# Performance work log

Hardware: AMD Instinct MI355X
Metric: run time of the kernel (lower is better)

The kernel has to match this reference:

```python
import jax, jax.numpy as jnp
import numpy as np

V, E, H, L = 32000, 512, 512, 3
HI = 2 * H  # expansion_factor = 2
B, S = 16, 2048


def setup_inputs() -> dict:
    key = jax.random.key(0)
    ks = jax.random.split(key, 9)
    x_source = jax.random.randint(ks[0], (B, S), 1, V)
    x_lengths = jax.random.randint(ks[1], (B,), 1, S + 1)
    x_lengths = x_lengths.at[0].set(S)  # ensure max(x_lengths) == S so truncation is static
    emb = jax.random.normal(ks[2], (V, E), jnp.float32) * 0.02
    emb = emb.at[0].set(0.0)  # padding_idx=0
    W_er = jax.random.normal(ks[3], (E, H), jnp.float32) / np.sqrt(E)
    b_er = jnp.zeros((H,), jnp.float32)
    W_hg_fwd = jax.random.normal(ks[4], (L, H, 2 * HI), jnp.float32) / np.sqrt(H)
    W_out_fwd = jax.random.normal(ks[5], (L, HI, H), jnp.float32) / np.sqrt(HI)
    W_hg_rev = jax.random.normal(ks[6], (L, H, 2 * HI), jnp.float32) / np.sqrt(H)
    W_out_rev = jax.random.normal(ks[7], (L, HI, H), jnp.float32) / np.sqrt(HI)
    return {"x_source": x_source, "x_lengths": x_lengths, "emb": emb,
            "W_er": W_er, "b_er": b_er,
            "W_hg_fwd": W_hg_fwd, "W_out_fwd": W_out_fwd,
            "W_hg_rev": W_hg_rev, "W_out_rev": W_out_rev}


def _log_g(x):
    # log of g(x) = where(x>=0, x+0.5, sigmoid(x)), computed stably in log space
    return jnp.where(x >= 0, jnp.log(jax.nn.relu(x) + 0.5), -jax.nn.softplus(-x))


def _mingru(x, W_hg, W_out):
    # x: [B,S,H] -> [B,S,H]; parallel minGRU via Heinsen associative scan in log space
    hidden, gate = jnp.split(x @ W_hg, 2, axis=-1)  # each [B,S,HI]
    log_coeffs = -jax.nn.softplus(gate)             # log(1 - z)
    log_values = -jax.nn.softplus(-gate) + _log_g(hidden)  # log z + log g(h~)
    a_star = jnp.cumsum(log_coeffs, axis=1)
    log_h = a_star + jax.lax.cumlogsumexp(log_values - a_star, axis=1)
    return jnp.exp(log_h) @ W_out


def _circ_shift_left(x, pad):
    # per-sample left rotation by pad[i]: cat([x[i, pad:], x[i, :pad]])
    Sl = x.shape[1]
    idx = (jnp.arange(Sl)[None, :] + pad[:, None]) % Sl  # [B,S]
    return jnp.take_along_axis(x, idx[:, :, None], axis=1)


def reference(x_source, x_lengths, emb, W_er, b_er, W_hg_fwd, W_out_fwd, W_hg_rev, W_out_rev):
    # seq_length = max(x_lengths) == S by construction, so truncation is identity
    x_emb = emb[x_source] @ W_er + b_er            # [B,S,H]
    pad = x_emb.shape[1] - x_lengths               # [B]
    rev = _circ_shift_left(jnp.flip(x_emb, axis=1), pad)
    h, hr = x_emb, rev
    for i in range(W_hg_fwd.shape[0]):
        h = _mingru(h, W_hg_fwd[i], W_out_fwd[i])
        hr = _mingru(hr, W_hg_rev[i], W_out_rev[i])
    hr = _circ_shift_left(jnp.flip(hr, axis=1), pad)
    out = jnp.concatenate([h, hr], axis=-1)        # [B,S,2H]
    # flattened gather in original == out[i, x_lengths[i]-1]
    seq_h = out[jnp.arange(out.shape[0]), x_lengths - 1]  # [B,2H]
    return out, seq_h
```

## Files before the change

### kernel.cpp

```cpp
#include <hip/hip_runtime.h>
#include <hip/hip_bf16.h>
#include <stdint.h>

#define S_LEN  2048
#define BATCH  16
#define HDIM   512
#define HIDIM  1024
#define NLAYER 3
#define SCAN_C 32
#define SCAN_T 64

typedef __hip_bfloat16 bf16;
typedef __attribute__((ext_vector_type(8))) short bf16x8;
typedef __attribute__((ext_vector_type(4))) float f32x4;
typedef unsigned int u32;

#define GLOAD16(gp, lp) __builtin_amdgcn_global_load_lds(                 \
    (const __attribute__((address_space(1))) void*)(gp),                  \
    (__attribute__((address_space(3))) void*)(lp), 16, 0, 0)

#define FENCE asm volatile("" ::: "memory")
#define BAR   do { FENCE; __builtin_amdgcn_s_barrier(); FENCE; } while (0)
#define VMCNT(n) asm volatile("s_waitcnt vmcnt(" #n ")" ::: "memory")

__global__ void probe_dtype(const unsigned short* __restrict__ w, int* __restrict__ flag)
{
  int cnt = 0;
  for (int i = threadIdx.x; i < 4096; i += 64) {
    unsigned short m = w[i] & 0x7FFF;
    if (m > 0x4080) cnt++;
  }
  for (int o = 32; o; o >>= 1) cnt += __shfl_down(cnt, o, 64);
  if (threadIdx.x == 0) *flag = (cnt > 64) ? 1 : 0;
}

__device__ __forceinline__ void av_calc(float hid, float gate, float& a, float& v) {
  a = 1.0f / (1.0f + __expf(gate));
  float z = 1.0f / (1.0f + __expf(-gate));
  float g = (hid >= 0.0f) ? (hid + 0.5f) : (1.0f / (1.0f + __expf(-hid)));
  v = z * g;
}

__device__ __forceinline__ short f2bs(float f) {
  bf16 h = (bf16)f;
  return *(short*)&h;
}

__device__ __forceinline__ bf16x8 pack8(float4 a, float4 b) {
  bf16x8 r;
  r[0] = f2bs(a.x); r[1] = f2bs(a.y); r[2] = f2bs(a.z); r[3] = f2bs(a.w);
  r[4] = f2bs(b.x); r[5] = f2bs(b.y); r[6] = f2bs(b.z); r[7] = f2bs(b.w);
  return r;
}


__device__ __forceinline__ void stage_half(const bf16* __restrict__ G, int row0, int ld,
                                           int kbase, char* lhalf, int tid)
{
  const int r  = tid >> 3;
  const int cc = (((tid & 7) ^ ((tid >> 3) & 7)) << 3);
  const bf16* g0 = G + (long)(row0 + r) * ld + (kbase + cc);
  char* l = lhalf + ((tid >> 6) << 10);
  GLOAD16(g0, l);
  GLOAD16(g0 + (long)64 * ld, l + 8192);
}

__device__ __forceinline__ bf16x8 frag_ld(const char* base, int Rl, int cb) {
  return *(const bf16x8*)(base + Rl * 128 + (cb ^ ((Rl & 7) << 4)));
}

__global__ __launch_bounds__(512, 2)
void gemm8(const bf16* __restrict__ A, const bf16* __restrict__ Bt,
           bf16* __restrict__ Cout, int K, int lda, int ldc)
{
  extern __shared__ char lds[];

  const int tid  = threadIdx.x;
  const int wave = tid >> 6;
  const int lane = tid & 63;
  const int wm = wave >> 2;
  const int wn = wave & 3;

  const u32 nwg = gridDim.x * gridDim.y;
  const u32 hb  = blockIdx.y * gridDim.x + blockIdx.x;
  const u32 cpx = nwg >> 3;
  const u32 swz = (hb & 7u) * cpx + (hb >> 3);
  const int m0 = (int)(swz / gridDim.x) * 256;
  const int n0 = (int)(swz % gridDim.x) * 256;

  char* A0 = lds;
  char* B0 = lds + 32768;
  char* A1 = lds + 65536;
  char* B1 = lds + 98304;

  const int fr = lane & 15;
  const int qh = lane >> 4;
  const int cqh = qh * 16;

  f32x4 acc[8][4];
#pragma unroll
  for (int i = 0; i < 8; i++)
#pragma unroll
    for (int j = 0; j < 4; j++)
#pragma unroll
      for (int r = 0; r < 4; r++) acc[i][j][r] = 0.0f;

  const int NJ = K >> 7;

  stage_half(A,  m0,       lda, 0,  A0,         tid);
  stage_half(A,  m0 + 128, lda, 0,  A0 + 16384, tid);
  stage_half(Bt, n0,       K,   0,  B0,         tid);
  stage_half(Bt, n0 + 128, K,   0,  B0 + 16384, tid);
  stage_half(Bt, n0,       K,   64, B1,         tid);
  stage_half(Bt, n0 + 128, K,   64, B1 + 16384, tid);
  VMCNT(4);
  BAR;

  for (int j = 0; j < NJ; ++j) {
    const int last = (j == NJ - 1);
    const int kO  = (2 * j + 1) * 64;
    const int kE2 = (2 * j + 2) * 64;
    const int kO2 = (2 * j + 3) * 64;

    {
      bf16x8 bfrag[4][2];
#pragma unroll
      for (int q = 0; q < 4; ++q) {
        if (q == 0) {
#pragma unroll
          for (int nt = 0; nt < 4; ++nt)
#pragma unroll
            for (int kk = 0; kk < 2; ++kk)
              bfrag[nt][kk] = frag_ld(B0, wn * 64 + nt * 16 + fr, kk * 64 + cqh);
        }
        bf16x8 afrag[2][2];
#pragma unroll
        for (int t = 0; t < 2; ++t)
#pragma unroll
          for (int kk = 0; kk < 2; ++kk)
            afrag[t][kk] = frag_ld(A0, wm * 128 + (2 * q + t) * 16 + fr, kk * 64 + cqh);

        if (q == 0) {
          stage_half(A, m0,       lda, kO, A1,         tid);
          stage_half(A, m0 + 128, lda, kO, A1 + 16384, tid);
        } else if (q == 1) {
          if (!last) stage_half(Bt, n0,       K, kE2, B0,         tid);
        } else if (q == 2) {
          if (!last) stage_half(Bt, n0 + 128, K, kE2, B0 + 16384, tid);
        }

        BAR;
        __builtin_amdgcn_s_setprio(1);
#pragma unroll
        for (int t = 0; t < 2; ++t)
#pragma unroll
          for (int nt = 0; nt < 4; ++nt)
#pragma unroll
            for (int kk = 0; kk < 2; ++kk)
              acc[2 * q + t][nt] = __builtin_amdgcn_mfma_f32_16x16x32_bf16(
                  afrag[t][kk], bfrag[nt][kk], acc[2 * q + t][nt], 0, 0, 0);
        __builtin_amdgcn_s_setprio(0);
        if (q == 3) {
          if (last) { VMCNT(0); } else { VMCNT(4); }
        }
        BAR;
      }
    }

    {
      bf16x8 bfrag[4][2];
#pragma unroll
      for (int q = 0; q < 4; ++q) {
        if (q == 0) {
#pragma unroll
          for (int nt = 0; nt < 4; ++nt)
#pragma unroll
            for (int kk = 0; kk < 2; ++kk)
              bfrag[nt][kk] = frag_ld(B1, wn * 64 + nt * 16 + fr, kk * 64 + cqh);
        }
        bf16x8 afrag[2][2];
#pragma unroll
        for (int t = 0; t < 2; ++t)
#pragma unroll
          for (int kk = 0; kk < 2; ++kk)
            afrag[t][kk] = frag_ld(A1, wm * 128 + (2 * q + t) * 16 + fr, kk * 64 + cqh);

        if (!last) {
          if (q == 0)      stage_half(A,  m0,       lda, kE2, A0,         tid);
          else if (q == 1) stage_half(A,  m0 + 128, lda, kE2, A0 + 16384, tid);
          else if (q == 2) stage_half(Bt, n0,       K,   kO2, B1,         tid);
          else             stage_half(Bt, n0 + 128, K,   kO2, B1 + 16384, tid);
        }

        BAR;
        __builtin_amdgcn_s_setprio(1);
#pragma unroll
        for (int t = 0; t < 2; ++t)
#pragma unroll
          for (int nt = 0; nt < 4; ++nt)
#pragma unroll
            for (int kk = 0; kk < 2; ++kk)
              acc[2 * q + t][nt] = __builtin_amdgcn_mfma_f32_16x16x32_bf16(
                  afrag[t][kk], bfrag[nt][kk], acc[2 * q + t][nt], 0, 0, 0);
        __builtin_amdgcn_s_setprio(0);
        if (q == 3 && !last) { VMCNT(4); }
        BAR;
      }
    }
  }

  const int orow = qh * 4;
#pragma unroll
  for (int mt = 0; mt < 8; ++mt) {
#pragma unroll
    for (int nt = 0; nt < 4; ++nt) {
      int gr = m0 + wm * 128 + mt * 16 + orow;
      int gc = n0 + wn * 64 + nt * 16 + fr;
#pragma unroll
      for (int r = 0; r < 4; ++r)
        Cout[(long)(gr + r) * ldc + gc] = (bf16)acc[mt][nt][r];
    }
  }
}

template<int GATHER, int BIAS>
__global__ __launch_bounds__(256, 2)
void gemm_mfma(const void* __restrict__ Av, const bf16* __restrict__ Bt,
               bf16* __restrict__ Cout, const float* __restrict__ bias,
               const int* __restrict__ gidx, const int* __restrict__ flag,
               int M, int N, int K, int lda, int ldc)
{
  __shared__ bf16 As[128 * 32];
  __shared__ bf16 Bs[128 * 32];

  const int tid  = threadIdx.x;
  const int wave = tid >> 6;
  const int lane = tid & 63;
  const int m0 = blockIdx.y * 128;
  const int n0 = blockIdx.x * 128;

  const int seg0 = wave * 2, seg1 = seg0 + 1;
  const int lr = lane >> 2;
  const int ck = (lane & 3) * 8;
  const int rA0 = seg0 * 16 + lr;
  const int rA1 = seg1 * 16 + lr;

  const int af = GATHER ? *flag : 0;

  long ga0 = GATHER ? (long)gidx[m0 + rA0] : (long)(m0 + rA0);
  long ga1 = GATHER ? (long)gidx[m0 + rA1] : (long)(m0 + rA1);
  const bf16*  hA0 = (const bf16*)Av + ga0 * (long)lda + ck;
  const bf16*  hA1 = (const bf16*)Av + ga1 * (long)lda + ck;
  const float* qA0 = (const float*)Av + ga0 * (long)lda + ck;
  const float* qA1 = (const float*)Av + ga1 * (long)lda + ck;
  const bf16*  pB0 = Bt + (long)(n0 + rA0) * K + ck;
  const bf16*  pB1 = Bt + (long)(n0 + rA1) * K + ck;

  bf16* lA0 = &As[seg0 * 512 + lane * 8];
  bf16* lA1 = &As[seg1 * 512 + lane * 8];
  bf16* lB0 = &Bs[seg0 * 512 + lane * 8];
  bf16* lB1 = &Bs[seg1 * 512 + lane * 8];

  f32x4 acc[4][4];
#pragma unroll
  for (int i = 0; i < 4; i++)
#pragma unroll
    for (int j = 0; j < 4; j++)
#pragma unroll
      for (int r = 0; r < 4; r++) acc[i][j][r] = 0.0f;

  const int mBase = (wave >> 1) * 64;
  const int nBase = (wave & 1) * 64;
  const int fr = lane & 15;
  const int fq = (lane >> 4) * 8;

  for (int k0 = 0; k0 < K; k0 += 32) {
    bf16x8 va0, va1;
    if (GATHER && af) {
      float4 a0 = *(const float4*)(qA0 + k0);
      float4 a1 = *(const float4*)(qA0 + k0 + 4);
      float4 b0 = *(const float4*)(qA1 + k0);
      float4 b1 = *(const float4*)(qA1 + k0 + 4);
      va0 = pack8(a0, a1);
      va1 = pack8(b0, b1);
    } else {
      va0 = *(const bf16x8*)(hA0 + k0);
      va1 = *(const bf16x8*)(hA1 + k0);
    }
    bf16x8 vb0 = *(const bf16x8*)(pB0 + k0);
    bf16x8 vb1 = *(const bf16x8*)(pB1 + k0);
    __syncthreads();
    *(bf16x8*)lA0 = va0;
    *(bf16x8*)lA1 = va1;
    *(bf16x8*)lB0 = vb0;
    *(bf16x8*)lB1 = vb1;
    __syncthreads();

    bf16x8 afr[4], bfr[4];
#pragma unroll
    for (int mt = 0; mt < 4; mt++)
      afr[mt] = *(const bf16x8*)&As[(mBase + mt * 16 + fr) * 32 + fq];
#pragma unroll
    for (int nt = 0; nt < 4; nt++)
      bfr[nt] = *(const bf16x8*)&Bs[(nBase + nt * 16 + fr) * 32 + fq];

#pragma unroll
    for (int mt = 0; mt < 4; mt++)
#pragma unroll
      for (int nt = 0; nt < 4; nt++)
        acc[mt][nt] = __builtin_amdgcn_mfma_f32_16x16x32_bf16(afr[mt], bfr[nt], acc[mt][nt], 0, 0, 0);
  }

  const int orow = (lane >> 4) * 4;
  const int ocol = lane & 15;
#pragma unroll
  for (int mt = 0; mt < 4; mt++) {
#pragma unroll
    for (int nt = 0; nt < 4; nt++) {
      int gr = m0 + mBase + mt * 16 + orow;
      int gc = n0 + nBase + nt * 16 + ocol;
      float bv = BIAS ? bias[gc] : 0.0f;
#pragma unroll
      for (int r = 0; r < 4; r++) {
        float v = acc[mt][nt][r] + bv;
        Cout[(long)(gr + r) * ldc + gc] = (bf16)v;
      }
    }
  }
}

__global__ __launch_bounds__(256)
void transpose_conv(const void* __restrict__ in, bf16* __restrict__ out,
                    const int* __restrict__ flag, int R, int C)
{
  __shared__ float tile[32][33];
  int f = *flag;
  int x = blockIdx.x * 32 + threadIdx.x;
  int yb = blockIdx.y * 32;
#pragma unroll
  for (int i = threadIdx.y; i < 32; i += 8) {
    long idx = (long)(yb + i) * C + x;
    tile[i][threadIdx.x] = f ? ((const float*)in)[idx] : (float)((const bf16*)in)[idx];
  }
  __syncthreads();
  int x2 = yb + threadIdx.x;
  int y2b = blockIdx.x * 32;
#pragma unroll
  for (int i = threadIdx.y; i < 32; i += 8)
    out[(long)(y2b + i) * R + x2] = (bf16)tile[threadIdx.x][i];
}

__global__ __launch_bounds__(256)
void transpose_conv2(const void* __restrict__ in32, const void* __restrict__ in16,
                     bf16* __restrict__ out, const int* __restrict__ flag, int R, int C)
{
  __shared__ float tile[32][33];
  int f = *flag;
  int x = blockIdx.x * 32 + threadIdx.x;
  int yb = blockIdx.y * 32;
#pragma unroll
  for (int i = threadIdx.y; i < 32; i += 8) {
    long idx = (long)(yb + i) * C + x;
    tile[i][threadIdx.x] = f ? ((const float*)in32)[idx] : (float)((const bf16*)in16)[idx];
  }
  __syncthreads();
  int x2 = yb + threadIdx.x;
  int y2b = blockIdx.x * 32;
#pragma unroll
  for (int i = threadIdx.y; i < 32; i += 8)
    out[(long)(y2b + i) * R + x2] = (bf16)tile[threadIdx.x][i];
}

__global__ __launch_bounds__(256)
void conv_to_f32(const void* __restrict__ in, float* __restrict__ out,
                 const int* __restrict__ flag, int n)
{
  int i = blockIdx.x * blockDim.x + threadIdx.x;
  if (i >= n) return;
  out[i] = (*flag) ? ((const float*)in)[i] : (float)((const bf16*)in)[i];
}

__global__ __launch_bounds__(256)
void scan_pass1(const bf16* __restrict__ HG, float* __restrict__ Ab, float* __restrict__ Pb)
{
  int tid = blockIdx.x * blockDim.x + threadIdx.x;
  int c  = tid & (HIDIM - 1);
  int bj = tid >> 10;
  int j  = bj & (SCAN_C - 1);
  int b  = bj >> 5;
  const bf16* base = HG + ((long)(b * S_LEN + j * SCAN_T)) * 2048 + c;
  float A = 1.0f, P = 0.0f;
#pragma unroll 4
  for (int t = 0; t < SCAN_T; t++) {
    float hid = (float)base[(long)t * 2048];
    float gt  = (float)base[(long)t * 2048 + 1024];
    float a, v; av_calc(hid, gt, a, v);
    A *= a;
    P = fmaf(a, P, v);
  }
  Ab[tid] = A;
  Pb[tid] = P;
}

__global__ __launch_bounds__(256)
void scan_pass2(const float* __restrict__ Ab, float* __restrict__ Pb)
{
  int tid = blockIdx.x * blockDim.x + threadIdx.x;
  int c = tid & (HIDIM - 1);
  int b = tid >> 10;
  float h = 0.0f;
  for (int j = 0; j < SCAN_C; j++) {
    long i = ((long)(b * SCAN_C + j) << 10) + c;
    float A = Ab[i];
    float P = Pb[i];
    Pb[i] = h;
    h = fmaf(A, h, P);
  }
}

__global__ __launch_bounds__(256)
void scan_pass3(bf16* __restrict__ HG, const float* __restrict__ Pb)
{
  int tid = blockIdx.x * blockDim.x + threadIdx.x;
  int c  = tid & (HIDIM - 1);
  int bj = tid >> 10;
  int j  = bj & (SCAN_C - 1);
  int b  = bj >> 5;
  bf16* base = HG + ((long)(b * S_LEN + j * SCAN_T)) * 2048 + c;
  float h = Pb[tid];
#pragma unroll 4
  for (int t = 0; t < SCAN_T; t++) {
    float hid = (float)base[(long)t * 2048];
    float gt  = (float)base[(long)t * 2048 + 1024];
    float a, v; av_calc(hid, gt, a, v);
    h = fmaf(a, h, v);
    base[(long)t * 2048] = (bf16)h;
  }
}

__global__ __launch_bounds__(256)
void rev_build(const bf16* __restrict__ X, bf16* __restrict__ X2, const int* __restrict__ lens)
{
  int bt = blockIdx.x;
  int b = bt >> 11;
  int t = bt & (S_LEN - 1);
  int pad = S_LEN - lens[b];
  int src = S_LEN - 1 - ((t + pad) & (S_LEN - 1));
  const u32* s = (const u32*)(X + (long)(b * S_LEN + src) * HDIM);
  u32* d = (u32*)(X2 + (long)(b * S_LEN + t) * HDIM);
  d[threadIdx.x] = s[threadIdx.x];
}

__global__ __launch_bounds__(256)
void finalize_out(const bf16* __restrict__ X, const bf16* __restrict__ X2,
                  const int* __restrict__ lens, const int* __restrict__ flag,
                  void* __restrict__ out)
{
  int bt = blockIdx.x;
  int b = bt >> 11;
  int t = bt & (S_LEN - 1);
  int pad = S_LEN - lens[b];
  int src = S_LEN - 1 - ((t + pad) & (S_LEN - 1));
  const bf16* sf = X  + (long)(b * S_LEN + t) * HDIM;
  const bf16* sr = X2 + (long)(b * S_LEN + src) * HDIM;
  long ro = (long)(b * S_LEN + t) * 1024;
  if (*flag) {
    float* d = (float*)out + ro;
    for (int c = threadIdx.x; c < 512; c += 256) {
      d[c]       = (float)sf[c];
      d[512 + c] = (float)sr[c];
    }
  } else {
    bf16* d = (bf16*)out + ro;
    for (int c = threadIdx.x; c < 512; c += 256) {
      d[c]       = sf[c];
      d[512 + c] = sr[c];
    }
  }
}

__global__ __launch_bounds__(256)
void seq_out_k(const bf16* __restrict__ X, const bf16* __restrict__ X2,
               const int* __restrict__ lens, const int* __restrict__ flag,
               void* __restrict__ out)
{
  int b = blockIdx.x;
  int t = lens[b] - 1;
  const bf16* sf = X  + (long)(b * S_LEN + t) * HDIM;
  const bf16* sr = X2 + (long)(b * S_LEN + 0) * HDIM;
  long off = (long)BATCH * S_LEN * 1024 + (long)b * 1024;
  if (*flag) {
    float* d = (float*)out + off;
    for (int c = threadIdx.x; c < 512; c += 256) {
      d[c]       = (float)sf[c];
      d[512 + c] = (float)sr[c];
    }
  } else {
    bf16* d = (bf16*)out + off;
    for (int c = threadIdx.x; c < 512; c += 256) {
      d[c]       = sf[c];
      d[512 + c] = sr[c];
    }
  }
}

extern "C" void kernel_launch(void* const* d_in, const int* in_sizes, int n_in,
                              void* d_out, int out_size, void* d_ws, size_t ws_size,
                              hipStream_t stream)
{
  (void)in_sizes; (void)n_in; (void)out_size;
  const int* x_source = (const int*)d_in[0];
  const int* x_len    = (const int*)d_in[1];
  const void* emb     = d_in[2];
  const void* W_er    = d_in[3];
  const void* b_er    = d_in[4];
  const void* W_hg[2]  = { d_in[5], d_in[7] };
  const void* W_out[2] = { d_in[6], d_in[8] };

  char* ws = (char*)d_ws;
  size_t off = 0;
  auto alloc = [&](size_t bytes) -> char* {
    char* p = ws + off;
    off += (bytes + 255) & ~(size_t)255;
    return p;
  };
  auto a256 = [](size_t b) -> size_t { return (b + 255) & ~(size_t)255; };

  int*   flag = (int*)  alloc(256);
  float* berF = (float*)alloc(512 * 4);
  bf16*  WerT = (bf16*) alloc((size_t)512 * 512 * 2);
  bf16*  X    = (bf16*) alloc((size_t)BATCH * S_LEN * HDIM * 2);
  bf16*  X2   = (bf16*) alloc((size_t)BATCH * S_LEN * HDIM * 2);
  bf16* WhgT[2][NLAYER];
  bf16* WoutT[2][NLAYER];
  for (int d = 0; d < 2; d++)
    for (int l = 0; l < NLAYER; l++) {
      WhgT[d][l]  = (bf16*)alloc((size_t)2048 * 512 * 2);
      WoutT[d][l] = (bf16*)alloc((size_t)512 * 1024 * 2);
    }

  size_t fixedEnd = off;
  int bch = 16;
  while (bch > 1) {
    size_t need = fixedEnd
      + a256((size_t)bch * S_LEN * 2048 * 2)
      + 2 * a256((size_t)bch * SCAN_C * HIDIM * 4);
    if (need <= ws_size) break;
    bch >>= 1;
  }
  bf16*  HG = (bf16*) alloc((size_t)bch * S_LEN * 2048 * 2);
  float* Ab = (float*)alloc((size_t)bch * SCAN_C * HIDIM * 4);
  float* Pb = (float*)alloc((size_t)bch * SCAN_C * HIDIM * 4);

  probe_dtype<<<1, 64, 0, stream>>>((const unsigned short*)emb, flag);

  conv_to_f32<<<2, 256, 0, stream>>>(b_er, berF, flag, 512);
  dim3 tb(32, 8);
  transpose_conv<<<dim3(16, 16), tb, 0, stream>>>(W_er, WerT, flag, 512, 512);
  for (int d = 0; d < 2; d++)
    for (int l = 0; l < NLAYER; l++) {
      const char* hg32 = (const char*)W_hg[d] + (size_t)l * 512 * 2048 * 4;
      const char* hg16 = (const char*)W_hg[d] + (size_t)l * 512 * 2048 * 2;
      const char* wo32 = (const char*)W_out[d] + (size_t)l * 1024 * 512 * 4;
      const char* wo16 = (const char*)W_out[d] + (size_t)l * 1024 * 512 * 2;
      transpose_conv2<<<dim3(2048 / 32, 512 / 32), tb, 0, stream>>>(hg32, hg16, WhgT[d][l], flag, 512, 2048);
      transpose_conv2<<<dim3(512 / 32, 1024 / 32), tb, 0, stream>>>(wo32, wo16, WoutT[d][l], flag, 1024, 512);
    }

  gemm_mfma<1, 1><<<dim3(4, (BATCH * S_LEN) / 128), 256, 0, stream>>>(
      emb, WerT, X, berF, x_source, flag, BATCH * S_LEN, 512, 512, 512, 512);

  rev_build<<<BATCH * S_LEN, 256, 0, stream>>>(X, X2, x_len);

  for (int d = 0; d < 2; d++) {
    bf16* Xd = d ? X2 : X;
    for (int l = 0; l < NLAYER; l++) {
      for (int cb = 0; cb < BATCH / bch; cb++) {
        bf16* Ain = Xd + (size_t)cb * bch * S_LEN * HDIM;
        int Mrows = bch * S_LEN;
        gemm8<<<dim3(2048 / 256, Mrows / 256), 512, 131072, stream>>>(
            Ain, WhgT[d][l], HG, 512, 512, 2048);
        int nthr = bch * SCAN_C * HIDIM;
        scan_pass1<<<nthr / 256, 256, 0, stream>>>(HG, Ab, Pb);
        scan_pass2<<<(bch * HIDIM) / 256, 256, 0, stream>>>(Ab, Pb);
        scan_pass3<<<nthr / 256, 256, 0, stream>>>(HG, Pb);
        gemm8<<<dim3(512 / 256, Mrows / 256), 512, 131072, stream>>>(
            HG, WoutT[d][l], Ain, 1024, 2048, 512);
      }
    }
  }

  finalize_out<<<BATCH * S_LEN, 256, 0, stream>>>(X, X2, x_len, flag, d_out);
  seq_out_k<<<BATCH, 256, 0, stream>>>(X, X2, x_len, flag, d_out);
}
```

Before: 1.777 ms.

## Batch forward and reverse directions into single GEMM and scan launches

The gemm8 kernel now takes two A/B/C pointer sets and picks one per block by row offset, so the forward and reverse minGRU stacks of a layer run together in one launch over 32 sequences. When workspace allows, this halves the number of GEMM and scan launches and doubles the grid size of each, which should improve occupancy, especially for the narrow output GEMM. The HG workspace doubles in size, and the MFMA loop order is also changed to iterate over k first. It falls back to per-direction chunks if workspace is insufficient.

After: 1.756 ms. No clear change (-1.2%).

```diff
diff --git a/kernel.cpp b/kernel.cpp
--- a/kernel.cpp
+++ b/kernel.cpp
@@ -70,8 +70,10 @@
 }
 
 __global__ __launch_bounds__(512, 2)
-void gemm8(const bf16* __restrict__ A, const bf16* __restrict__ Bt,
-           bf16* __restrict__ Cout, int K, int lda, int ldc)
+void gemm8(const bf16* __restrict__ Aa, const bf16* __restrict__ Aa2,
+           const bf16* __restrict__ Bta, const bf16* __restrict__ Bta2,
+           bf16* __restrict__ Ca, bf16* __restrict__ Ca2,
+           int K, int lda, int ldc, int mHalf)
 {
   extern __shared__ char lds[];
 
@@ -85,8 +87,13 @@
   const u32 hb  = blockIdx.y * gridDim.x + blockIdx.x;
   const u32 cpx = nwg >> 3;
   const u32 swz = (hb & 7u) * cpx + (hb >> 3);
-  const int m0 = (int)(swz / gridDim.x) * 256;
-  const int n0 = (int)(swz % gridDim.x) * 256;
+  const int m0g = (int)(swz / gridDim.x) * 256;
+  const int n0  = (int)(swz % gridDim.x) * 256;
+
+  const bf16* A  = (m0g >= mHalf) ? Aa2 : Aa;
+  const bf16* Bt = (m0g >= mHalf) ? Bta2 : Bta;
+  bf16*       Cout = (m0g >= mHalf) ? Ca2 : Ca;
+  const int m0 = (m0g >= mHalf) ? (m0g - mHalf) : m0g;
 
   char* A0 = lds;
   char* B0 = lds + 32768;
@@ -152,11 +159,11 @@
         BAR;
         __builtin_amdgcn_s_setprio(1);
 #pragma unroll
-        for (int t = 0; t < 2; ++t)
+        for (int kk = 0; kk < 2; ++kk)
 #pragma unroll
           for (int nt = 0; nt < 4; ++nt)
 #pragma unroll
-            for (int kk = 0; kk < 2; ++kk)
+            for (int t = 0; t < 2; ++t)
               acc[2 * q + t][nt] = __builtin_amdgcn_mfma_f32_16x16x32_bf16(
                   afrag[t][kk], bfrag[nt][kk], acc[2 * q + t][nt], 0, 0, 0);
         __builtin_amdgcn_s_setprio(0);
@@ -195,11 +202,11 @@
         BAR;
         __builtin_amdgcn_s_setprio(1);
 #pragma unroll
-        for (int t = 0; t < 2; ++t)
+        for (int kk = 0; kk < 2; ++kk)
 #pragma unroll
           for (int nt = 0; nt < 4; ++nt)
 #pragma unroll
-            for (int kk = 0; kk < 2; ++kk)
+            for (int t = 0; t < 2; ++t)
               acc[2 * q + t][nt] = __builtin_amdgcn_mfma_f32_16x16x32_bf16(
                   afrag[t][kk], bfrag[nt][kk], acc[2 * q + t][nt], 0, 0, 0);
         __builtin_amdgcn_s_setprio(0);
@@ -540,17 +547,17 @@
     }
 
   size_t fixedEnd = off;
-  int bch = 16;
-  while (bch > 1) {
+  int bchv = 32;
+  while (bchv > 1) {
     size_t need = fixedEnd
-      + a256((size_t)bch * S_LEN * 2048 * 2)
-      + 2 * a256((size_t)bch * SCAN_C * HIDIM * 4);
+      + a256((size_t)bchv * S_LEN * 2048 * 2)
+      + 2 * a256((size_t)bchv * SCAN_C * HIDIM * 4);
     if (need <= ws_size) break;
-    bch >>= 1;
-  }
-  bf16*  HG = (bf16*) alloc((size_t)bch * S_LEN * 2048 * 2);
-  float* Ab = (float*)alloc((size_t)bch * SCAN_C * HIDIM * 4);
-  float* Pb = (float*)alloc((size_t)bch * SCAN_C * HIDIM * 4);
+    bchv >>= 1;
+  }
+  bf16*  HG = (bf16*) alloc((size_t)bchv * S_LEN * 2048 * 2);
+  float* Ab = (float*)alloc((size_t)bchv * SCAN_C * HIDIM * 4);
+  float* Pb = (float*)alloc((size_t)bchv * SCAN_C * HIDIM * 4);
 
   probe_dtype<<<1, 64, 0, stream>>>((const unsigned short*)emb, flag);
 
@@ -572,21 +579,34 @@
 
   rev_build<<<BATCH * S_LEN, 256, 0, stream>>>(X, X2, x_len);
 
-  for (int d = 0; d < 2; d++) {
-    bf16* Xd = d ? X2 : X;
-    for (int l = 0; l < NLAYER; l++) {
-      for (int cb = 0; cb < BATCH / bch; cb++) {
-        bf16* Ain = Xd + (size_t)cb * bch * S_LEN * HDIM;
-        int Mrows = bch * S_LEN;
-        gemm8<<<dim3(2048 / 256, Mrows / 256), 512, 131072, stream>>>(
-            Ain, WhgT[d][l], HG, 512, 512, 2048);
-        int nthr = bch * SCAN_C * HIDIM;
-        scan_pass1<<<nthr / 256, 256, 0, stream>>>(HG, Ab, Pb);
-        scan_pass2<<<(bch * HIDIM) / 256, 256, 0, stream>>>(Ab, Pb);
-        scan_pass3<<<nthr / 256, 256, 0, stream>>>(HG, Pb);
-        gemm8<<<dim3(512 / 256, Mrows / 256), 512, 131072, stream>>>(
-            HG, WoutT[d][l], Ain, 1024, 2048, 512);
+  const int nchunk = 32 / bchv;
+  for (int l = 0; l < NLAYER; l++) {
+    for (int cb = 0; cb < nchunk; cb++) {
+      const int s0    = cb * bchv;
+      const int Mrows = bchv * S_LEN;
+      int mHalf;
+      bf16 *Xa, *Xa2; const bf16 *Bh, *Bh2, *Bo, *Bo2;
+      if (bchv == 32) {
+        mHalf = 16 * S_LEN;
+        Xa  = X;  Xa2 = X2;
+        Bh  = WhgT[0][l];  Bh2 = WhgT[1][l];
+        Bo  = WoutT[0][l]; Bo2 = WoutT[1][l];
+      } else {
+        const int dir = s0 >> 4;
+        mHalf = Mrows;
+        Xa  = (dir ? X2 : X) + (size_t)(s0 & 15) * S_LEN * HDIM;
+        Xa2 = Xa;
+        Bh  = WhgT[dir][l];  Bh2 = Bh;
+        Bo  = WoutT[dir][l]; Bo2 = Bo;
       }
+      gemm8<<<dim3(2048 / 256, Mrows / 256), 512, 131072, stream>>>(
+          Xa, Xa2, Bh, Bh2, HG, HG + (size_t)mHalf * 2048, 512, 512, 2048, mHalf);
+      int nthr = bchv * SCAN_C * HIDIM;
+      scan_pass1<<<nthr / 256, 256, 0, stream>>>(HG, Ab, Pb);
+      scan_pass2<<<(bchv * HIDIM) / 256, 256, 0, stream>>>(Ab, Pb);
+      scan_pass3<<<nthr / 256, 256, 0, stream>>>(HG, Pb);
+      gemm8<<<dim3(512 / 256, Mrows / 256), 512, 131072, stream>>>(
+          HG, HG + (size_t)mHalf * 2048, Bo, Bo2, Xa, Xa2, 1024, 2048, 512, mHalf);
     }
   }
 
```
